# Kernel tuning notes

Hardware: AMD Instinct MI355X
Metric: run time of the kernel (lower is better)

## Reference

```python
import jax, jax.numpy as jnp
import numpy as np
from jax import lax

H = 16        # linear_num_key_heads == linear_num_value_heads
DK = 64       # linear_key_head_dim
DV = 128      # linear_value_head_dim
HID = 2048    # hidden_size
KCONV = 4     # linear_conv_kernel_dim
SEQ = 2048
KEY_DIM = H * DK       # 1024
VAL_DIM = H * DV       # 2048
CONV_DIM = 2 * KEY_DIM + VAL_DIM  # 4096


def _l2norm(x, eps=1e-6):
    return x * lax.rsqrt(jnp.sum(x * x, axis=-1, keepdims=True) + eps)


def setup_inputs() -> dict:
    key = jax.random.key(0)
    ks = jax.random.split(key, 10)
    s = 0.02
    return {
        "hidden_states": jax.random.normal(ks[0], (1, SEQ, HID), jnp.float32),
        "in_proj_qkv": jax.random.normal(ks[1], (CONV_DIM, HID), jnp.float32) * s,
        "in_proj_a": jax.random.normal(ks[2], (H, HID), jnp.float32) * s,
        "in_proj_b": jax.random.normal(ks[3], (H, HID), jnp.float32) * s,
        "in_proj_z": jax.random.normal(ks[4], (VAL_DIM, HID), jnp.float32) * s,
        "conv_w": jax.random.normal(ks[5], (CONV_DIM, 1, KCONV), jnp.float32) * 0.5,
        "A_log": jax.random.normal(ks[6], (H,), jnp.float32) * 0.5,
        "dt_bias": jnp.ones((H,), jnp.float32),
        "norm_w": jnp.ones((DV,), jnp.float32),
        "out_proj": jax.random.normal(ks[7], (HID, VAL_DIM), jnp.float32) * s,
        "is_prefill": 1,
    }


def reference(hidden_states, in_proj_qkv, in_proj_a, in_proj_b, in_proj_z,
              conv_w, A_log, dt_bias, norm_w, out_proj, is_prefill):
    b, s, _ = hidden_states.shape  # b == 1
    # QKV projection: (1, S, CONV_DIM)
    mixed = jnp.einsum('bsh,oh->bso', hidden_states, in_proj_qkv)
    # Depthwise causal conv1d over time (left pad K-1), then SiLU
    x = mixed.transpose(0, 2, 1)  # (1, C, S)
    x = lax.conv_general_dilated(
        x, conv_w, window_strides=(1,), padding=[(KCONV - 1, 0)],
        feature_group_count=CONV_DIM, dimension_numbers=('NCH', 'OIH', 'NCH'))
    mixed = jax.nn.silu(x).transpose(0, 2, 1)[0]  # (S, CONV_DIM), squeeze batch

    q = mixed[:, :KEY_DIM].reshape(s, H, DK)
    k = mixed[:, KEY_DIM:2 * KEY_DIM].reshape(s, H, DK)
    v = mixed[:, 2 * KEY_DIM:].reshape(s, H, DV)

    hs = hidden_states[0]  # (S, HID)
    a = hs @ in_proj_a.T                      # (S, H)
    g = -jnp.exp(A_log) * jax.nn.softplus(a + dt_bias)  # (S, H) log-decay
    beta = jax.nn.sigmoid(hs @ in_proj_b.T)   # (S, H)
    z = (hs @ in_proj_z.T).reshape(s, H, DV)  # (S, H, DV)

    q = _l2norm(q) * (1.0 / np.sqrt(DK))
    k = _l2norm(k)

    # Delta-rule recurrence; prefill -> zero initial state
    S0 = jnp.zeros((H, DK, DV), jnp.float32)

    def step(St, inp):
        q_t, k_t, v_t, g_t, beta_t = inp
        St = St * jnp.exp(g_t)[:, None, None]            # decay
        kv_mem = jnp.einsum('hk,hkv->hv', k_t, St)       # read
        delta = (v_t - kv_mem) * beta_t[:, None]         # gated error
        St = St + jnp.einsum('hk,hv->hkv', k_t, delta)   # rank-1 update
        o_t = jnp.einsum('hk,hkv->hv', q_t, St)          # query read
        return St, o_t

    _, core = lax.scan(step, S0, (q, k, v, g, beta))  # core: (S, H, DV)

    # Gated RMSNorm over DV, then SiLU(z) gate
    var = jnp.mean(core * core, axis=-1, keepdims=True)
    core = core * lax.rsqrt(var + 1e-6) * norm_w
    core = core * jax.nn.silu(z)
    core = core.reshape(1, s, VAL_DIM)
    return jnp.einsum('bsv,hv->bsh', core, out_proj)
```

## Files before the change

### kernel.cpp

```cpp
#include <hip/hip_runtime.h>
#include <stdint.h>


#define SEQ 2048
#define HIDDEN 2048
#define NH 16
#define DKv 64
#define DVv 128
#define KEY_DIM 1024
#define VAL_DIM 2048
#define CONV_DIM 4096

typedef __bf16 bf16;
typedef unsigned short u16;
typedef __attribute__((ext_vector_type(8))) __bf16 bf16x8;
typedef __attribute__((ext_vector_type(4))) __bf16 bf16x4;
typedef __attribute__((ext_vector_type(4))) float f32x4;

#define AS1 __attribute__((address_space(1)))
#define AS3 __attribute__((address_space(3)))
#define GLDS16(src, dst) __builtin_amdgcn_global_load_lds((AS1 const void*)(src), (AS3 void*)(dst), 16, 0, 0)

__device__ __forceinline__ float b2f(u16 u) {
  union { unsigned int i; float f; } c; c.i = ((unsigned int)u) << 16; return c.f;
}
__device__ __forceinline__ float sigmoidf_(float x) { return 1.0f / (1.0f + __expf(-x)); }

__global__ void detect_dtype(const u16* __restrict__ p, unsigned* __restrict__ flag) {
  int lane = threadIdx.x;
  int cnt = 0;
  for (int w = lane; w < 2048; w += 64) {
    unsigned e = (p[2 * w] >> 7) & 0xFF;
    if (e < 64) cnt++;
  }
  cnt += __shfl_xor(cnt, 1);  cnt += __shfl_xor(cnt, 2);  cnt += __shfl_xor(cnt, 4);
  cnt += __shfl_xor(cnt, 8);  cnt += __shfl_xor(cnt, 16); cnt += __shfl_xor(cnt, 32);
  if (lane == 0) *flag = (cnt > 64) ? 1u : 0u;
}

__global__ __launch_bounds__(256)
void cvt_bf16(const void* __restrict__ src, bf16* __restrict__ dst, long n,
              const unsigned* __restrict__ flagp) {
  long i = ((long)blockIdx.x * 256 + threadIdx.x) * 8;
  if (i >= n) return;
  if (*flagp) {
    const f32x4* s = (const f32x4*)((const float*)src + i);
    f32x4 a = s[0], b = s[1];
    bf16x8 o;
#pragma unroll
    for (int j = 0; j < 4; ++j) { o[j] = (bf16)a[j]; o[4 + j] = (bf16)b[j]; }
    *(bf16x8*)(dst + i) = o;
  } else {
    *(bf16x8*)(dst + i) = *(const bf16x8*)((const bf16*)src + i);
  }
}

template<bool F32OUT>
__global__ __launch_bounds__(256, 2)
void gemm_nt(const void* __restrict__ Araw, const void* __restrict__ Braw,
             void* __restrict__ Cv, int N, int K,
             const unsigned* __restrict__ flagp, int useA, int useB) {
  __shared__ __align__(16) bf16 As[128 * 32];
  __shared__ __align__(16) bf16 Bs[128 * 32];
  const bool f32g = (*flagp != 0);
  const bool fA = useA && f32g;
  const bool fB = useB && f32g;
  const int tid  = threadIdx.x;
  const int lane = tid & 63;
  const int wv   = tid >> 6;
  const int wm   = (wv & 1) << 6;
  const int wn   = (wv >> 1) << 6;
  const long bm  = (long)blockIdx.y * 128;
  const long bn  = (long)blockIdx.x * 128;

  f32x4 acc[4][4] = {};

  for (int k0 = 0; k0 < K; k0 += 32) {
#pragma unroll
    for (int it = 0; it < 2; ++it) {
      int e   = (it * 256 + tid) * 8;
      int row = e >> 5;
      int col = e & 31;
      long offA = (bm + row) * (long)K + (k0 + col);
      long offB = (bn + row) * (long)K + (k0 + col);
      if (fA) {
        const float* g = (const float*)Araw + offA;
        f32x4 u0 = *(const f32x4*)g, u1 = *(const f32x4*)(g + 4);
        bf16x8 bv;
#pragma unroll
        for (int j = 0; j < 4; ++j) { bv[j] = (bf16)u0[j]; bv[4 + j] = (bf16)u1[j]; }
        *(bf16x8*)&As[e] = bv;
      } else {
        const bf16* g = (const bf16*)Araw + offA;
        GLDS16(g, &As[e]);
      }
      if (fB) {
        const float* g = (const float*)Braw + offB;
        f32x4 u0 = *(const f32x4*)g, u1 = *(const f32x4*)(g + 4);
        bf16x8 bv;
#pragma unroll
        for (int j = 0; j < 4; ++j) { bv[j] = (bf16)u0[j]; bv[4 + j] = (bf16)u1[j]; }
        *(bf16x8*)&Bs[e] = bv;
      } else {
        const bf16* g = (const bf16*)Braw + offB;
        GLDS16(g, &Bs[e]);
      }
    }
    __syncthreads();

    const bf16x8* As8 = (const bf16x8*)As;
    const bf16x8* Bs8 = (const bf16x8*)Bs;
    const int r = lane & 15, q = lane >> 4;
    bf16x8 af[4], bfr[4];
#pragma unroll
    for (int i = 0; i < 4; ++i) af[i]  = As8[(wm + i * 16 + r) * 4 + q];
#pragma unroll
    for (int j = 0; j < 4; ++j) bfr[j] = Bs8[(wn + j * 16 + r) * 4 + q];
#pragma unroll
    for (int i = 0; i < 4; ++i)
#pragma unroll
      for (int j = 0; j < 4; ++j)
        acc[i][j] = __builtin_amdgcn_mfma_f32_16x16x32_bf16(af[i], bfr[j], acc[i][j], 0, 0, 0);
    __syncthreads();
  }

  const int r = lane & 15, q = lane >> 4;
#pragma unroll
  for (int i = 0; i < 4; ++i)
#pragma unroll
    for (int j = 0; j < 4; ++j) {
      long row = bm + wm + i * 16 + q * 4;
      long col = bn + wn + j * 16 + r;
#pragma unroll
      for (int rr = 0; rr < 4; ++rr) {
        if constexpr (F32OUT) ((float*)Cv)[(row + rr) * N + col] = acc[i][j][rr];
        else                  ((bf16*)Cv)[(row + rr) * N + col] = (bf16)acc[i][j][rr];
      }
    }
}

__device__ void gemm_body_bf16(char* smemc, const bf16* __restrict__ A,
                               const bf16* __restrict__ B, bf16* __restrict__ C,
                               int N, int K, int bx, int by, int tid) {
  bf16* As = (bf16*)smemc;
  bf16* Bs = (bf16*)(smemc + 8192);
  const int lane = tid & 63;
  const int wv = tid >> 6, wm = (wv & 1) << 6, wn = (wv >> 1) << 6;
  const long bm = (long)by * 128, bn = (long)bx * 128;
  f32x4 acc[4][4] = {};
  for (int k0 = 0; k0 < K; k0 += 32) {
#pragma unroll
    for (int it = 0; it < 2; ++it) {
      int e = (it * 256 + tid) * 8;
      int row = e >> 5, col = e & 31;
      const bf16* gA = A + (bm + row) * (long)K + k0 + col;
      const bf16* gB = B + (bn + row) * (long)K + k0 + col;
      GLDS16(gA, &As[e]);
      GLDS16(gB, &Bs[e]);
    }
    __syncthreads();
    const bf16x8* As8 = (const bf16x8*)As;
    const bf16x8* Bs8 = (const bf16x8*)Bs;
    const int r = lane & 15, q = lane >> 4;
    bf16x8 af[4], bfr[4];
#pragma unroll
    for (int i = 0; i < 4; ++i) af[i]  = As8[(wm + i * 16 + r) * 4 + q];
#pragma unroll
    for (int j = 0; j < 4; ++j) bfr[j] = Bs8[(wn + j * 16 + r) * 4 + q];
#pragma unroll
    for (int i = 0; i < 4; ++i)
#pragma unroll
      for (int j = 0; j < 4; ++j)
        acc[i][j] = __builtin_amdgcn_mfma_f32_16x16x32_bf16(af[i], bfr[j], acc[i][j], 0, 0, 0);
    __syncthreads();
  }
  const int r = lane & 15, q = lane >> 4;
#pragma unroll
  for (int i = 0; i < 4; ++i)
#pragma unroll
    for (int j = 0; j < 4; ++j) {
      long row = bm + wm + i * 16 + q * 4;
      long col = bn + wn + j * 16 + r;
#pragma unroll
      for (int rr = 0; rr < 4; ++rr)
        C[(row + rr) * (long)N + col] = (bf16)acc[i][j][rr];
    }
}

__global__ __launch_bounds__(256)
void proj_ab(const void* __restrict__ hsr, const void* __restrict__ War,
             const void* __restrict__ Wbr, const void* __restrict__ A_logr,
             const void* __restrict__ dtbr,
             float* __restrict__ eg, float* __restrict__ bet,
             float* __restrict__ gb,
             const unsigned* __restrict__ flagp) {
  const bool f32g = (*flagp != 0);
  const int s = blockIdx.x;
  const int t = threadIdx.x;
  const int o = t & 31;
  const int part = t >> 5;
  const int h = o & 15;
  const int kbeg = part * 256;
  float a0 = 0.f, a1 = 0.f;
  if (f32g) {
    const f32x4* x4 = (const f32x4*)((const float*)hsr + (long)s * HIDDEN + kbeg);
    const f32x4* w4 = (const f32x4*)((const float*)((o < 16) ? War : Wbr) + (long)h * HIDDEN + kbeg);
#pragma unroll 8
    for (int k4 = 0; k4 < 64; ++k4) {
      f32x4 xv = x4[k4], wv = w4[k4];
      a0 += xv[0] * wv[0] + xv[1] * wv[1];
      a1 += xv[2] * wv[2] + xv[3] * wv[3];
    }
  } else {
    const bf16x8* x8 = (const bf16x8*)((const bf16*)hsr + (long)s * HIDDEN + kbeg);
    const bf16x8* w8 = (const bf16x8*)((const bf16*)((o < 16) ? War : Wbr) + (long)h * HIDDEN + kbeg);
#pragma unroll 8
    for (int k8 = 0; k8 < 32; ++k8) {
      bf16x8 xv = x8[k8], wv = w8[k8];
#pragma unroll
      for (int j = 0; j < 4; ++j) a0 += (float)xv[j] * (float)wv[j];
#pragma unroll
      for (int j = 4; j < 8; ++j) a1 += (float)xv[j] * (float)wv[j];
    }
  }
  __shared__ float red[256];
  red[t] = a0 + a1;
  __syncthreads();
  if (t < 32) {
    float a = 0.f;
#pragma unroll
    for (int p = 0; p < 8; ++p) a += red[t + p * 32];
    const int hh = t & 15;
    if (t < 16) {
      float alog = f32g ? ((const float*)A_logr)[hh] : b2f(((const u16*)A_logr)[hh]);
      float dtb  = f32g ? ((const float*)dtbr)[hh]   : b2f(((const u16*)dtbr)[hh]);
      float xx = a + dtb;
      float sp = fmaxf(xx, 0.f) + log1pf(__expf(-fabsf(xx)));
      float gg = -__expf(alog) * sp;
      if (gb) gb[(long)s * NH + hh] = gg;
      eg[(long)s * NH + hh] = __expf(gg);
    } else {
      bet[(long)s * NH + hh] = sigmoidf_(a);
    }
  }
}

__global__ __launch_bounds__(256)
void conv_norm(const bf16* __restrict__ mixed, const void* __restrict__ convwr,
               bf16* __restrict__ qbuf, bf16* __restrict__ kbuf, bf16* __restrict__ vbuf,
               const unsigned* __restrict__ flagp) {
  const bool f32g = (*flagp != 0);
  const int s = blockIdx.x;
  const int c = blockIdx.y * 256 + threadIdx.x;
  float w0, w1, w2, w3;
  if (f32g) {
    const float* wp = (const float*)convwr + (long)c * 4;
    w0 = wp[0]; w1 = wp[1]; w2 = wp[2]; w3 = wp[3];
  } else {
    const u16* wp = (const u16*)convwr + (long)c * 4;
    w0 = b2f(wp[0]); w1 = b2f(wp[1]); w2 = b2f(wp[2]); w3 = b2f(wp[3]);
  }
  float acc = w3 * (float)mixed[(long)s * CONV_DIM + c];
  if (s >= 1) acc += w2 * (float)mixed[(long)(s - 1) * CONV_DIM + c];
  if (s >= 2) acc += w1 * (float)mixed[(long)(s - 2) * CONV_DIM + c];
  if (s >= 3) acc += w0 * (float)mixed[(long)(s - 3) * CONV_DIM + c];
  float y = acc * sigmoidf_(acc);
  if (c < 2 * KEY_DIM) {
    float ss = y * y;
    ss += __shfl_xor(ss, 1);  ss += __shfl_xor(ss, 2);  ss += __shfl_xor(ss, 4);
    ss += __shfl_xor(ss, 8);  ss += __shfl_xor(ss, 16); ss += __shfl_xor(ss, 32);
    float scale = rsqrtf(ss + 1e-6f);
    if (c < KEY_DIM) scale *= 0.125f;
    y *= scale;
  }
  if (c < KEY_DIM)            qbuf[(long)s * KEY_DIM + c] = (bf16)y;
  else if (c < 2 * KEY_DIM)   kbuf[(long)s * KEY_DIM + (c - KEY_DIM)] = (bf16)y;
  else                        vbuf[(long)s * VAL_DIM + (c - 2 * KEY_DIM)] = (bf16)y;
}

template<int CTRL>
__device__ __forceinline__ float dpp_add(float x) {
  int y = __builtin_amdgcn_update_dpp(0, __float_as_int(x), CTRL, 0xF, 0xF, true);
  return x + __int_as_float(y);
}
__device__ __forceinline__ float dpp_sum16(float x) {
  x = dpp_add<0xB1>(x);
  x = dpp_add<0x4E>(x);
  x = dpp_add<0x141>(x);
  x = dpp_add<0x140>(x);
  return x;
}

__global__ __launch_bounds__(256, 2)
void fused_scan(const bf16* __restrict__ qbuf, const bf16* __restrict__ kbuf,
                const bf16* __restrict__ vbuf, const float* __restrict__ eg,
                const float* __restrict__ bet, bf16* __restrict__ core,
                const bf16* __restrict__ hsb, const bf16* __restrict__ wzb,
                bf16* __restrict__ zbuf, const void* __restrict__ woutr,
                bf16* __restrict__ woutb, const unsigned* __restrict__ flagp,
                int nScan, int nGemm) {
  __shared__ __align__(16) char smem[16384];
  const int t = threadIdx.x;
  const int b = blockIdx.x;

  if (b < nScan) {
    const int h  = b >> 3;
    const int vg = (b & 7) * 16;
    const int g  = t >> 4;
    const int L  = t & 15;
    bf16*  kqs = (bf16*)smem;
    bf16*  vts = (bf16*)(smem + 8192);
    float* ets = (float*)(smem + 9216);
    float* bts = (float*)(smem + 9344);

#define STAGE(buf, s0)                                                          \
    {                                                                           \
      int byte = t * 16;                                                        \
      const bf16* src;                                                          \
      if (byte < 2048) {                                                        \
        int row = byte >> 7, el = (byte & 127) >> 1;                            \
        src = kbuf + (long)((s0) + row) * KEY_DIM + h * DKv + el;               \
      } else {                                                                  \
        int b2 = byte - 2048;                                                   \
        int row = b2 >> 7, el = (b2 & 127) >> 1;                                \
        src = qbuf + (long)((s0) + row) * KEY_DIM + h * DKv + el;               \
      }                                                                         \
      GLDS16(src, smem + (buf) * 4096 + byte);                                  \
      if (t < 32) {                                                             \
        int row = t >> 1, el = (t & 1) * 8;                                     \
        const bf16* vsrc = vbuf + (long)((s0) + row) * VAL_DIM + h * DVv + vg + el; \
        GLDS16(vsrc, smem + 8192 + (buf) * 512 + t * 16);                       \
      }                                                                         \
    }

    float er = 0.f, br = 0.f;
    if (t < 16)      er = eg[(long)t * NH + h];
    else if (t < 32) br = bet[(long)(t - 16) * NH + h];
    STAGE(0, 0);
    if (t < 16)      ets[t] = er;
    else if (t < 32) bts[t - 16] = br;
    __syncthreads();

    float S0 = 0.f, S1 = 0.f, S2 = 0.f, S3 = 0.f;
    for (int tile = 0; tile < 128; ++tile) {
      const int buf = tile & 1, nb = buf ^ 1;
      if (tile < 127) {
        STAGE(nb, (tile + 1) * 16);
        if (t < 16)      er = eg[(long)((tile + 1) * 16 + t) * NH + h];
        else if (t < 32) br = bet[(long)((tile + 1) * 16 + (t - 16)) * NH + h];
      }
      const bf16*  ktb = kqs + buf * 2048;
      const bf16*  qtb = ktb + 1024;
      const bf16*  vtb = vts + buf * 256;
      const float* etb = ets + buf * 16;
      const float* btb = bts + buf * 16;
      const long sbase = (long)tile * 16;

      bf16x4 kR[2], qR[2];
      float  vR[2], eR[2], bR[2];
      kR[0] = *(const bf16x4*)(ktb + 0 * 64 + L * 4);
      qR[0] = *(const bf16x4*)(qtb + 0 * 64 + L * 4);
      vR[0] = (float)vtb[0 * 16 + g];  eR[0] = etb[0];  bR[0] = btb[0];
      kR[1] = *(const bf16x4*)(ktb + 1 * 64 + L * 4);
      qR[1] = *(const bf16x4*)(qtb + 1 * 64 + L * 4);
      vR[1] = (float)vtb[1 * 16 + g];  eR[1] = etb[1];  bR[1] = btb[1];
#pragma unroll
      for (int s = 0; s < 16; ++s) {
        const int sl = s & 1;
        bf16x4 kk = kR[sl], qq = qR[sl];
        float vv = vR[sl], ee = eR[sl], bb = bR[sl];
        if (s < 14) {
          const int s2 = s + 2;
          kR[sl] = *(const bf16x4*)(ktb + s2 * 64 + L * 4);
          qR[sl] = *(const bf16x4*)(qtb + s2 * 64 + L * 4);
          vR[sl] = (float)vtb[s2 * 16 + g];
          eR[sl] = etb[s2];  bR[sl] = btb[s2];
        }
        float ebt = ee * bb, vbt = vv * bb;
        float k0 = (float)kk[0], k1 = (float)kk[1], k2 = (float)kk[2], k3 = (float)kk[3];
        float D0 = S0 * ee, D1 = S1 * ee, D2 = S2 * ee, D3 = S3 * ee;
        float p = (k0 * S0 + k1 * S1) + (k2 * S2 + k3 * S3);
        p = dpp_sum16(p);
        float delta = vbt - ebt * p;
        S0 = fmaf(k0, delta, D0); S1 = fmaf(k1, delta, D1);
        S2 = fmaf(k2, delta, D2); S3 = fmaf(k3, delta, D3);
        float q0 = (float)qq[0], q1 = (float)qq[1], q2 = (float)qq[2], q3 = (float)qq[3];
        float o = (q0 * S0 + q1 * S1) + (q2 * S2 + q3 * S3);
        o = dpp_sum16(o);
        if (L == 0) core[(sbase + s) * VAL_DIM + h * DVv + vg + g] = (bf16)o;
      }
      if (tile < 127) {
        if (t < 16)      ets[nb * 16 + t] = er;
        else if (t < 32) bts[nb * 16 + (t - 16)] = br;
      }
      __syncthreads();
    }
#undef STAGE
  } else if (b < nScan + nGemm) {
    int gb = b - nScan;
    gemm_body_bf16(smem, hsb, wzb, zbuf, VAL_DIM, HIDDEN, gb & 15, gb >> 4, t);
  } else {
    long i = ((long)(b - nScan - nGemm) * 256 + t) * 8;
    if (i < (long)HIDDEN * VAL_DIM) {
      if (*flagp) {
        const f32x4* s = (const f32x4*)((const float*)woutr + i);
        f32x4 a = s[0], c = s[1];
        bf16x8 o;
#pragma unroll
        for (int j = 0; j < 4; ++j) { o[j] = (bf16)a[j]; o[4 + j] = (bf16)c[j]; }
        *(bf16x8*)(woutb + i) = o;
      } else {
        *(bf16x8*)(woutb + i) = *(const bf16x8*)((const bf16*)woutr + i);
      }
    }
  }
}


__global__ __launch_bounds__(256, 2)
void chunk_a(const bf16* __restrict__ kbuf, const bf16* __restrict__ vbuf,
             const float* __restrict__ gbuf, const float* __restrict__ betp,
             bf16* __restrict__ dloc, bf16* __restrict__ whig, bf16* __restrict__ wlog,
             const bf16* __restrict__ hsb, const bf16* __restrict__ wzb,
             bf16* __restrict__ zbuf, const void* __restrict__ woutr,
             bf16* __restrict__ woutb, const unsigned* __restrict__ flagp) {
  __shared__ __align__(16) char smem[25600];
  const int t = threadIdx.x;
  const int b = blockIdx.x;
  if (b < 512) {
    const int c = b >> 4, h = b & 15;
    bf16*  Ks   = (bf16*)smem;
    float* At   = (float*)(smem + 8192);
    float* cumS = (float*)(smem + 24576);
    float* bS   = (float*)(smem + 24832);
    float* dS   = (float*)(smem + 25088);
#pragma unroll
    for (int it = 0; it < 2; ++it) {
      int byte = (it * 256 + t) * 16;
      int row = byte >> 7, col = (byte & 127) >> 1;
      const bf16* src = kbuf + (long)(c * 64 + row) * KEY_DIM + h * DKv + col;
      GLDS16(src, smem + byte);
    }
    if (t < 64) {
      float cc = gbuf[(long)(c * 64 + t) * NH + h];
#pragma unroll
      for (int d = 1; d < 64; d <<= 1) { float y = __shfl_up(cc, d); if (t >= d) cc += y; }
      cumS[t] = cc;
      dS[t] = __expf(cc);
      bS[t] = betp[(long)(c * 64 + t) * NH + h];
    }
    {
      f32x4 z = {0.f, 0.f, 0.f, 0.f};
#pragma unroll
      for (int i = 0; i < 4; ++i) ((f32x4*)At)[t * 4 + i] = z;
    }
    __syncthreads();
    {
      const int lane = t & 63, wv = t >> 6;
      const int r = lane & 15, q = lane >> 4;
      const bf16x8* Ks8 = (const bf16x8*)Ks;
#pragma unroll
      for (int n = 0; n < 4; ++n) {
        f32x4 acc = {0.f, 0.f, 0.f, 0.f};
#pragma unroll
        for (int kk = 0; kk < 2; ++kk) {
          bf16x8 af  = Ks8[(wv * 16 + r) * 8 + kk * 4 + q];
          bf16x8 bfv = Ks8[(n  * 16 + r) * 8 + kk * 4 + q];
          acc = __builtin_amdgcn_mfma_f32_16x16x32_bf16(af, bfv, acc, 0, 0, 0);
        }
        const int i = n * 16 + r;
#pragma unroll
        for (int rr = 0; rr < 4; ++rr) {
          const int tr = wv * 16 + q * 4 + rr;
          if (i < tr)
            At[i * 64 + tr] = bS[tr] * __expf(cumS[tr] - cumS[i]) * acc[rr];
        }
      }
    }
    __syncthreads();
    if (t < 192) {
      float x[64];
      const long base = ((long)(c * 16 + h)) * 64;
      if (t < 128) {
#pragma unroll
        for (int s = 0; s < 64; ++s)
          x[s] = bS[s] * (float)vbuf[(long)(c * 64 + s) * VAL_DIM + h * DVv + t];
      } else {
        const int k = t - 128;
#pragma unroll
        for (int s = 0; s < 64; ++s)
          x[s] = bS[s] * dS[s] * (float)Ks[s * 64 + k];
      }
#pragma unroll
      for (int s = 0; s < 64; ++s) {
        const float val = x[s];
        const f32x4* row4 = (const f32x4*)(At + s * 64);
#pragma unroll
        for (int qd = (s >> 2); qd < 16; ++qd) {
          f32x4 a4 = row4[qd];
          x[qd * 4 + 0] = fmaf(-a4[0], val, x[qd * 4 + 0]);
          x[qd * 4 + 1] = fmaf(-a4[1], val, x[qd * 4 + 1]);
          x[qd * 4 + 2] = fmaf(-a4[2], val, x[qd * 4 + 2]);
          x[qd * 4 + 3] = fmaf(-a4[3], val, x[qd * 4 + 3]);
        }
      }
      if (t < 128) {
#pragma unroll
        for (int s = 0; s < 64; ++s)
          dloc[(base + s) * 128 + t] = (bf16)x[s];
      } else {
        const int k = t - 128;
        const long wb = base * 64;
#pragma unroll
        for (int s = 0; s < 64; ++s) {
          float v = -x[s];
          bf16 hh = (bf16)v;
          whig[wb + s * 64 + k] = hh;
          wlog[wb + s * 64 + k] = (bf16)(v - (float)hh);
        }
      }
    }
  } else if (b < 768) {
    int gb = b - 512;
    gemm_body_bf16(smem, hsb, wzb, zbuf, VAL_DIM, HIDDEN, gb & 15, gb >> 4, t);
  } else {
    long i = ((long)(b - 768) * 256 + t) * 8;
    if (i < (long)HIDDEN * VAL_DIM) {
      if (*flagp) {
        const f32x4* s = (const f32x4*)((const float*)woutr + i);
        f32x4 a = s[0], cc = s[1];
        bf16x8 o;
#pragma unroll
        for (int j = 0; j < 4; ++j) { o[j] = (bf16)a[j]; o[4 + j] = (bf16)cc[j]; }
        *(bf16x8*)(woutb + i) = o;
      } else {
        *(bf16x8*)(woutb + i) = *(const bf16x8*)((const bf16*)woutr + i);
      }
    }
  }
}

__global__ __launch_bounds__(256, 1)
void chunk_b(const bf16* __restrict__ qbuf, const bf16* __restrict__ kbuf,
             const float* __restrict__ gbuf, const bf16* __restrict__ dloc,
             const bf16* __restrict__ whig, const bf16* __restrict__ wlog,
             bf16* __restrict__ dTg, bf16* __restrict__ o1g) {
  __shared__ __align__(16) char smem[123904];
  bf16* Wh  = (bf16*)(smem);
  bf16* Wl  = (bf16*)(smem + 16384);
  bf16* Qs  = (bf16*)(smem + 32768);
  bf16* Ks  = (bf16*)(smem + 49152);
  bf16* Dls = (bf16*)(smem + 65536);
  bf16* KT  = (bf16*)(smem + 81920);
  bf16* Shi = (bf16*)(smem + 90112);
  bf16* Slo = (bf16*)(smem + 98304);
  bf16* Dth = (bf16*)(smem + 106496);
  bf16* Dtl = (bf16*)(smem + 114688);
  float* fSb = (float*)(smem + 122880);
  float* dSb = (float*)(smem + 123392);

  const int t = threadIdx.x;
  const int h = blockIdx.x >> 1, vhalf = blockIdx.x & 1;
  const int lane = t & 63, w = t >> 6;
  const int r = lane & 15, q = lane >> 4;
  const int tb = w * 16 + q * 4;

  auto stage = [&](int bb, int cc) {
    const long c16h = (long)(cc * 16 + h);
#pragma unroll
    for (int it = 0; it < 2; ++it) {
      int p = it * 256 + t;
      int row = p >> 3, g = p & 7;
      int sg = ((g ^ (row & 7)) << 3);
      GLDS16(whig + c16h * 4096 + row * 64 + sg, (char*)Wh + bb * 8192 + p * 16);
      GLDS16(wlog + c16h * 4096 + row * 64 + sg, (char*)Wl + bb * 8192 + p * 16);
      GLDS16(qbuf + (long)(cc * 64 + row) * KEY_DIM + h * DKv + sg, (char*)Qs + bb * 8192 + p * 16);
      GLDS16(kbuf + (long)(cc * 64 + row) * KEY_DIM + h * DKv + (g << 3), (char*)Ks + bb * 8192 + p * 16);
      GLDS16(dloc + (c16h * 64 + row) * 128 + vhalf * 64 + sg, (char*)Dls + bb * 8192 + p * 16);
    }
  };
  auto prefix = [&](int bb, int cc) {
    if (t < 64) {
      float cs = gbuf[(long)(cc * 64 + t) * NH + h];
#pragma unroll
      for (int d = 1; d < 64; d <<= 1) { float y = __shfl_up(cs, d); if (t >= d) cs += y; }
      float tot = __shfl(cs, 63);
      fSb[bb * 64 + t] = __expf(tot - cs);
      dSb[bb * 64 + t] = __expf(cs);
    }
  };

  {
    f32x4 z = {0.f, 0.f, 0.f, 0.f};
    ((f32x4*)Shi)[t] = z; ((f32x4*)Shi)[t + 256] = z;
    ((f32x4*)Slo)[t] = z; ((f32x4*)Slo)[t + 256] = z;
  }
  stage(0, 0);
  prefix(0, 0);
  f32x4 Sacc[4] = {};

  for (int c = 0; c < 32; ++c) {
    const int buf = c & 1, nb = buf ^ 1;
    __syncthreads();
    const bf16* wh = Wh + buf * 4096;
    const bf16* wl = Wl + buf * 4096;
    const bf16* qs = Qs + buf * 4096;
    const bf16* ks = Ks + buf * 4096;
    const bf16* dl = Dls + buf * 4096;
    const float* fS = fSb + buf * 64;
    const float* dS = dSb + buf * 64;
    const long gch = (long)(c * 16 + h) * 8192 + (long)(vhalf * 64) * 64;

    if (c < 31) {
      const int k = lane;
#pragma unroll
      for (int ii = 0; ii < 16; ++ii) {
        const int i = w * 16 + ii;
        const int pg = (i >> 3) ^ (k & 7);
        KT[k * 64 + pg * 8 + (i & 7)] = ks[i * 64 + k];
      }
    }

    float fs4[4], ds4[4];
#pragma unroll
    for (int rr = 0; rr < 4; ++rr) { fs4[rr] = fS[tb + rr]; ds4[rr] = dS[tb + rr]; }

    bf16x8 wahi[2], walo[2], qa[2];
#pragma unroll
    for (int kk = 0; kk < 2; ++kk) {
      const int row = w * 16 + r;
      const int g = (kk * 4 + q) ^ (row & 7);
      wahi[kk] = *(const bf16x8*)(wh + row * 64 + g * 8);
      walo[kk] = *(const bf16x8*)(wl + row * 64 + g * 8);
      qa[kk]   = *(const bf16x8*)(qs + row * 64 + g * 8);
    }

#pragma unroll
    for (int n = 0; n < 4; ++n) {
      const int vrow = n * 16 + r;
      bf16x8 sh[2], sl[2];
#pragma unroll
      for (int kk = 0; kk < 2; ++kk) {
        const int g = (kk * 4 + q) ^ (vrow & 7);
        sh[kk] = *(const bf16x8*)(Shi + vrow * 64 + g * 8);
        sl[kk] = *(const bf16x8*)(Slo + vrow * 64 + g * 8);
      }
      f32x4 da;
#pragma unroll
      for (int rr = 0; rr < 4; ++rr) {
        const int trow = tb + rr;
        const int pg = (vrow >> 3) ^ (trow & 7);
        da[rr] = (float)dl[trow * 64 + pg * 8 + (vrow & 7)];
      }
      f32x4 oa = {0.f, 0.f, 0.f, 0.f};
#pragma unroll
      for (int kk = 0; kk < 2; ++kk) {
        da = __builtin_amdgcn_mfma_f32_16x16x32_bf16(wahi[kk], sh[kk], da, 0, 0, 0);
        da = __builtin_amdgcn_mfma_f32_16x16x32_bf16(wahi[kk], sl[kk], da, 0, 0, 0);
        da = __builtin_amdgcn_mfma_f32_16x16x32_bf16(walo[kk], sh[kk], da, 0, 0, 0);
        oa = __builtin_amdgcn_mfma_f32_16x16x32_bf16(qa[kk],   sh[kk], oa, 0, 0, 0);
        oa = __builtin_amdgcn_mfma_f32_16x16x32_bf16(qa[kk],   sl[kk], oa, 0, 0, 0);
      }
      bf16x4 dpk, opk, fhk, flk;
#pragma unroll
      for (int rr = 0; rr < 4; ++rr) {
        float dv = da[rr];
        dpk[rr] = (bf16)dv;
        float p = fs4[rr] * dv;
        bf16 ph = (bf16)p;
        fhk[rr] = ph;
        flk[rr] = (bf16)(p - (float)ph);
        opk[rr] = (bf16)(ds4[rr] * oa[rr]);
      }
      *(bf16x4*)(dTg + gch + (long)vrow * 64 + tb) = dpk;
      *(bf16x4*)(o1g + gch + (long)vrow * 64 + tb) = opk;
      const int pg = (tb >> 3) ^ (vrow & 7);
      *(bf16x4*)(Dth + vrow * 64 + pg * 8 + (tb & 7)) = fhk;
      *(bf16x4*)(Dtl + vrow * 64 + pg * 8 + (tb & 7)) = flk;
    }

    __syncthreads();
    if (c < 31) {
      stage(nb, c + 1);
      prefix(nb, c + 1);
      const float dC = dS[63];
      bf16x8 dh[2], dlo[2];
#pragma unroll
      for (int kk = 0; kk < 2; ++kk) {
        const int vrow = w * 16 + r;
        const int g = (kk * 4 + q) ^ (vrow & 7);
        dh[kk]  = *(const bf16x8*)(Dth + vrow * 64 + g * 8);
        dlo[kk] = *(const bf16x8*)(Dtl + vrow * 64 + g * 8);
      }
#pragma unroll
      for (int n = 0; n < 4; ++n) {
        f32x4 sa;
#pragma unroll
        for (int rr = 0; rr < 4; ++rr) sa[rr] = dC * Sacc[n][rr];
        bf16x8 ktf[2];
#pragma unroll
        for (int kk = 0; kk < 2; ++kk) {
          const int krow = n * 16 + r;
          const int g = (kk * 4 + q) ^ (krow & 7);
          ktf[kk] = *(const bf16x8*)(KT + krow * 64 + g * 8);
        }
#pragma unroll
        for (int kk = 0; kk < 2; ++kk) {
          sa = __builtin_amdgcn_mfma_f32_16x16x32_bf16(dh[kk],  ktf[kk], sa, 0, 0, 0);
          sa = __builtin_amdgcn_mfma_f32_16x16x32_bf16(dlo[kk], ktf[kk], sa, 0, 0, 0);
        }
        Sacc[n] = sa;
        const int k = n * 16 + r;
#pragma unroll
        for (int rr = 0; rr < 4; ++rr) {
          const int v = tb + rr;
          float s = sa[rr];
          bf16 hh = (bf16)s;
          const int pg = (k >> 3) ^ (v & 7);
          Shi[v * 64 + pg * 8 + (k & 7)] = hh;
          Slo[v * 64 + pg * 8 + (k & 7)] = (bf16)(s - (float)hh);
        }
      }
    }
  }
}

__global__ __launch_bounds__(256, 2)
void chunk_c(const bf16* __restrict__ qbuf, const bf16* __restrict__ kbuf,
             const float* __restrict__ gbuf, const bf16* __restrict__ dTg,
             const bf16* __restrict__ o1g, bf16* __restrict__ core) {
  __shared__ __align__(16) char smem[57600];
  const int t = threadIdx.x;
  const int c = blockIdx.x >> 4, h = blockIdx.x & 15;
  const long c16h = (long)(c * 16 + h);
  bf16* Qs  = (bf16*)smem;
  bf16* Ksl = (bf16*)(smem + 8192);
  bf16* Pl  = (bf16*)(smem + 16384);
  const bf16* dT  = (const bf16*)(smem + 24576);
  const bf16* o1l = (const bf16*)(smem + 40960);
  float* cumS = (float*)(smem + 57344);

#pragma unroll
  for (int it = 0; it < 2; ++it) {
    int byte = (it * 256 + t) * 16;
    int row = byte >> 7, col = (byte & 127) >> 1;
    GLDS16(qbuf + (long)(c * 64 + row) * KEY_DIM + h * DKv + col, smem + byte);
    GLDS16(kbuf + (long)(c * 64 + row) * KEY_DIM + h * DKv + col, smem + 8192 + byte);
  }
#pragma unroll
  for (int it = 0; it < 4; ++it) {
    int byte = (it * 256 + t) * 16;
    GLDS16(dTg + c16h * 8192 + (byte >> 1), smem + 24576 + byte);
    GLDS16(o1g + c16h * 8192 + (byte >> 1), smem + 40960 + byte);
  }
  if (t < 64) {
    float cc = gbuf[(long)(c * 64 + t) * NH + h];
#pragma unroll
    for (int d = 1; d < 64; d <<= 1) { float y = __shfl_up(cc, d); if (t >= d) cc += y; }
    cumS[t] = cc;
  }
  __syncthreads();

  const int lane = t & 63, wv = t >> 6;
  const int r = lane & 15, q = lane >> 4;
  const bf16x8* Qs8 = (const bf16x8*)Qs;
  const bf16x8* Ks8 = (const bf16x8*)Ksl;

#pragma unroll
  for (int n = 0; n < 4; ++n) {
    f32x4 acc = {0.f, 0.f, 0.f, 0.f};
#pragma unroll
    for (int kk = 0; kk < 2; ++kk)
      acc = __builtin_amdgcn_mfma_f32_16x16x32_bf16(
          Qs8[(wv * 16 + r) * 8 + kk * 4 + q], Ks8[(n * 16 + r) * 8 + kk * 4 + q], acc, 0, 0, 0);
    const int i = n * 16 + r;
#pragma unroll
    for (int rr = 0; rr < 4; ++rr) {
      const int tr = wv * 16 + q * 4 + rr;
      Pl[tr * 64 + i] = (i <= tr) ? (bf16)(__expf(cumS[tr] - cumS[i]) * acc[rr]) : (bf16)0.0f;
    }
  }
  __syncthreads();

  {
    const bf16x8* Pl8 = (const bf16x8*)Pl;
    const bf16x8* dT8 = (const bf16x8*)dT;
    bf16x8 pf[2];
#pragma unroll
    for (int kk = 0; kk < 2; ++kk) pf[kk] = Pl8[(wv * 16 + r) * 8 + kk * 4 + q];
#pragma unroll
    for (int n = 0; n < 8; ++n) {
      const int v = n * 16 + r;
      f32x4 acc;
#pragma unroll
      for (int rr = 0; rr < 4; ++rr)
        acc[rr] = (float)o1l[v * 64 + (wv * 16 + q * 4 + rr)];
#pragma unroll
      for (int kk = 0; kk < 2; ++kk)
        acc = __builtin_amdgcn_mfma_f32_16x16x32_bf16(
            pf[kk], dT8[(n * 16 + r) * 8 + kk * 4 + q], acc, 0, 0, 0);
#pragma unroll
      for (int rr = 0; rr < 4; ++rr) {
        const int tr = wv * 16 + q * 4 + rr;
        core[(long)(c * 64 + tr) * VAL_DIM + h * DVv + v] = (bf16)acc[rr];
      }
    }
  }
}

__global__ __launch_bounds__(256)
void gate_norm(const bf16* __restrict__ core, const bf16* __restrict__ zb,
               const void* __restrict__ normwr, bf16* __restrict__ gated,
               const unsigned* __restrict__ flagp) {
  const bool f32g = (*flagp != 0);
  const int s  = blockIdx.x;
  const int t  = threadIdx.x;
  const int h  = t >> 4;
  const int li = t & 15;
  const long base = (long)s * VAL_DIM + h * DVv + li * 8;
  bf16x8 c8 = *(const bf16x8*)(core + base);
  bf16x8 z8 = *(const bf16x8*)(zb + base);
  float x[8], z[8], nw[8];
  float ss = 0.f;
#pragma unroll
  for (int j = 0; j < 8; ++j) { x[j] = (float)c8[j]; z[j] = (float)z8[j]; ss += x[j] * x[j]; }
  if (f32g) {
    const float* np_ = (const float*)normwr + li * 8;
#pragma unroll
    for (int j = 0; j < 8; ++j) nw[j] = np_[j];
  } else {
    const u16* np_ = (const u16*)normwr + li * 8;
#pragma unroll
    for (int j = 0; j < 8; ++j) nw[j] = b2f(np_[j]);
  }
  ss += __shfl_xor(ss, 1); ss += __shfl_xor(ss, 2);
  ss += __shfl_xor(ss, 4); ss += __shfl_xor(ss, 8);
  float scale = rsqrtf(ss * (1.f / 128.f) + 1e-6f);
#pragma unroll
  for (int j = 0; j < 8; ++j) {
    float y = x[j] * scale * nw[j];
    y *= z[j] * sigmoidf_(z[j]);
    gated[base + j] = (bf16)y;
  }
}

extern "C" void kernel_launch(void* const* d_in, const int* in_sizes, int n_in,
                              void* d_out, int out_size, void* d_ws, size_t ws_size,
                              hipStream_t stream) {
  char* ws = (char*)d_ws;
  const bool big = ws_size >= ((48u << 20) + (512u << 10));

  if (big) {
    bf16*  hsb   = (bf16*)ws;
    bf16*  wqkvb = (bf16*)(ws + (8u << 20));
    bf16*  wzb   = (bf16*)(ws + (8u << 20));
    bf16*  zbuf  = (bf16*)(ws + (16u << 20));
    bf16*  mixed = (bf16*)(ws + (24u << 20));
    bf16*  whig  = (bf16*)(ws + (24u << 20));
    bf16*  wlog  = (bf16*)(ws + (28u << 20));
    bf16*  woutb = (bf16*)(ws + (32u << 20));
    bf16*  qbuf  = (bf16*)(ws + (40u << 20));
    bf16*  kbuf  = (bf16*)(ws + (44u << 20));
    bf16*  gated = (bf16*)(ws + (40u << 20));
    bf16*  dTg   = (bf16*)ws;
    bf16*  o1g   = (bf16*)(ws + (8u << 20));
    float* egp  = (float*)(ws + (48u << 20));
    float* betp = (float*)(ws + (48u << 20) + (128u << 10));
    float* gbp  = (float*)(ws + (48u << 20) + (256u << 10));
    unsigned* flagp = (unsigned*)(ws + (48u << 20) + (384u << 10));
    bf16* vbuf  = (bf16*)d_out;
    bf16* dlocp = (bf16*)((char*)d_out + (8u << 20));
    bf16* corep = (bf16*)d_out;

    detect_dtype<<<1, 64, 0, stream>>>((const u16*)d_in[0], flagp);
    proj_ab<<<SEQ, 256, 0, stream>>>(d_in[0], d_in[2], d_in[3], d_in[6], d_in[7], egp, betp, gbp, flagp);
    cvt_bf16<<<(SEQ * HIDDEN) / 2048, 256, 0, stream>>>(d_in[0], hsb, (long)SEQ * HIDDEN, flagp);
    cvt_bf16<<<(CONV_DIM * HIDDEN) / 2048, 256, 0, stream>>>(d_in[1], wqkvb, (long)CONV_DIM * HIDDEN, flagp);
    gemm_nt<false><<<dim3(CONV_DIM / 128, SEQ / 128), 256, 0, stream>>>(hsb, wqkvb, mixed, CONV_DIM, HIDDEN, flagp, 0, 0);
    cvt_bf16<<<(VAL_DIM * HIDDEN) / 2048, 256, 0, stream>>>(d_in[4], wzb, (long)VAL_DIM * HIDDEN, flagp);
    conv_norm<<<dim3(SEQ, CONV_DIM / 256), 256, 0, stream>>>(mixed, d_in[5], qbuf, kbuf, vbuf, flagp);
    chunk_a<<<512 + 256 + 2048, 256, 0, stream>>>(kbuf, vbuf, gbp, betp, dlocp, whig, wlog,
                                                  hsb, wzb, zbuf, d_in[9], woutb, flagp);
    chunk_b<<<32, 256, 0, stream>>>(qbuf, kbuf, gbp, dlocp, whig, wlog, dTg, o1g);
    chunk_c<<<512, 256, 0, stream>>>(qbuf, kbuf, gbp, dTg, o1g, corep);
    gate_norm<<<SEQ, 256, 0, stream>>>(corep, zbuf, d_in[8], gated, flagp);
    gemm_nt<true><<<dim3(HIDDEN / 128, SEQ / 128), 256, 0, stream>>>(gated, woutb, d_out, HIDDEN, VAL_DIM, flagp, 0, 0);
  } else {
    bf16* mixed = (bf16*)ws;
    bf16* qbuf  = (bf16*)(ws + (16u << 20));
    bf16* kbuf  = (bf16*)(ws + (20u << 20));
    bf16* zbuf  = (bf16*)ws;
    bf16* corep = (bf16*)(ws + (8u << 20));
    bf16* gated = (bf16*)(ws + (16u << 20));
    float* egp  = (float*)(ws + (24u << 20));
    float* betp = (float*)(ws + (24u << 20) + (128u << 10));
    unsigned* flagp = (unsigned*)(ws + (24u << 20) + (256u << 10));
    bf16* vbuf  = (bf16*)d_out;

    detect_dtype<<<1, 64, 0, stream>>>((const u16*)d_in[0], flagp);
    proj_ab<<<SEQ, 256, 0, stream>>>(d_in[0], d_in[2], d_in[3], d_in[6], d_in[7], egp, betp, nullptr, flagp);
    gemm_nt<false><<<dim3(CONV_DIM / 128, SEQ / 128), 256, 0, stream>>>(d_in[0], d_in[1], mixed, CONV_DIM, HIDDEN, flagp, 1, 1);
    conv_norm<<<dim3(SEQ, CONV_DIM / 256), 256, 0, stream>>>(mixed, d_in[5], qbuf, kbuf, vbuf, flagp);
    gemm_nt<false><<<dim3(VAL_DIM / 128, SEQ / 128), 256, 0, stream>>>(d_in[0], d_in[4], zbuf, VAL_DIM, HIDDEN, flagp, 1, 1);
    fused_scan<<<128, 256, 0, stream>>>(qbuf, kbuf, vbuf, egp, betp, corep,
                                        nullptr, nullptr, nullptr, nullptr, nullptr, flagp,
                                        128, 0);
    gate_norm<<<SEQ, 256, 0, stream>>>(corep, zbuf, d_in[8], gated, flagp);
    gemm_nt<true><<<dim3(HIDDEN / 128, SEQ / 128), 256, 0, stream>>>(gated, d_in[9], d_out, HIDDEN, VAL_DIM, flagp, 0, 1);
  }
}
```

Baseline: 531.7 us.

## Precompute all chunk decay prefixes upfront, issue next-chunk staging earlier, batch LDS loads

```diff
diff --git a/kernel.cpp b/kernel.cpp
--- a/kernel.cpp
+++ b/kernel.cpp
@@ -545,7 +545,7 @@
              const float* __restrict__ gbuf, const bf16* __restrict__ dloc,
              const bf16* __restrict__ whig, const bf16* __restrict__ wlog,
              bf16* __restrict__ dTg, bf16* __restrict__ o1g) {
-  __shared__ __align__(16) char smem[123904];
+  __shared__ __align__(16) char smem[139264];
   bf16* Wh  = (bf16*)(smem);
   bf16* Wl  = (bf16*)(smem + 16384);
   bf16* Qs  = (bf16*)(smem + 32768);
@@ -556,8 +556,8 @@
   bf16* Slo = (bf16*)(smem + 98304);
   bf16* Dth = (bf16*)(smem + 106496);
   bf16* Dtl = (bf16*)(smem + 114688);
-  float* fSb = (float*)(smem + 122880);
-  float* dSb = (float*)(smem + 123392);
+  float* fSa = (float*)(smem + 122880);
+  float* dSa = (float*)(smem + 131072);
 
   const int t = threadIdx.x;
   const int h = blockIdx.x >> 1, vhalf = blockIdx.x & 1;
@@ -579,36 +579,41 @@
       GLDS16(dloc + (c16h * 64 + row) * 128 + vhalf * 64 + sg, (char*)Dls + bb * 8192 + p * 16);
     }
   };
-  auto prefix = [&](int bb, int cc) {
-    if (t < 64) {
-      float cs = gbuf[(long)(cc * 64 + t) * NH + h];
-#pragma unroll
-      for (int d = 1; d < 64; d <<= 1) { float y = __shfl_up(cs, d); if (t >= d) cs += y; }
+
+  {
+    float g8[8];
+#pragma unroll
+    for (int i = 0; i < 8; ++i)
+      g8[i] = gbuf[(long)((w * 8 + i) * 64 + lane) * NH + h];
+#pragma unroll
+    for (int i = 0; i < 8; ++i) {
+      float cs = g8[i];
+#pragma unroll
+      for (int d = 1; d < 64; d <<= 1) { float y = __shfl_up(cs, d); if (lane >= d) cs += y; }
       float tot = __shfl(cs, 63);
-      fSb[bb * 64 + t] = __expf(tot - cs);
-      dSb[bb * 64 + t] = __expf(cs);
-    }
-  };
-
+      fSa[(w * 8 + i) * 64 + lane] = __expf(tot - cs);
+      dSa[(w * 8 + i) * 64 + lane] = __expf(cs);
+    }
+  }
   {
     f32x4 z = {0.f, 0.f, 0.f, 0.f};
     ((f32x4*)Shi)[t] = z; ((f32x4*)Shi)[t + 256] = z;
     ((f32x4*)Slo)[t] = z; ((f32x4*)Slo)[t + 256] = z;
   }
   stage(0, 0);
-  prefix(0, 0);
   f32x4 Sacc[4] = {};
 
   for (int c = 0; c < 32; ++c) {
     const int buf = c & 1, nb = buf ^ 1;
     __syncthreads();
+    if (c < 31) stage(nb, c + 1);
     const bf16* wh = Wh + buf * 4096;
     const bf16* wl = Wl + buf * 4096;
     const bf16* qs = Qs + buf * 4096;
     const bf16* ks = Ks + buf * 4096;
     const bf16* dl = Dls + buf * 4096;
-    const float* fS = fSb + buf * 64;
-    const float* dS = dSb + buf * 64;
+    const float* fS = fSa + c * 64;
+    const float* dS = dSa + c * 64;
     const long gch = (long)(c * 16 + h) * 8192 + (long)(vhalf * 64) * 64;
 
     if (c < 31) {
@@ -634,43 +639,51 @@
       walo[kk] = *(const bf16x8*)(wl + row * 64 + g * 8);
       qa[kk]   = *(const bf16x8*)(qs + row * 64 + g * 8);
     }
+    bf16x8 sh[4][2], sl[4][2];
+#pragma unroll
+    for (int n = 0; n < 4; ++n)
+#pragma unroll
+      for (int kk = 0; kk < 2; ++kk) {
+        const int vrow = n * 16 + r;
+        const int g = (kk * 4 + q) ^ (vrow & 7);
+        sh[n][kk] = *(const bf16x8*)(Shi + vrow * 64 + g * 8);
+        sl[n][kk] = *(const bf16x8*)(Slo + vrow * 64 + g * 8);
+      }
+    float dl4[4][4];
+#pragma unroll
+    for (int n = 0; n < 4; ++n)
+#pragma unroll
+      for (int rr = 0; rr < 4; ++rr) {
+        const int vrow = n * 16 + r, trow = tb + rr;
+        const int pg = (vrow >> 3) ^ (trow & 7);
+        dl4[n][rr] = (float)dl[trow * 64 + pg * 8 + (vrow & 7)];
+      }
+
+    f32x4 da[4] = {}, oa[4] = {};
+#pragma unroll
+    for (int n = 0; n < 4; ++n)
+#pragma unroll
+      for (int kk = 0; kk < 2; ++kk) {
+        da[n] = __builtin_amdgcn_mfma_f32_16x16x32_bf16(wahi[kk], sh[n][kk], da[n], 0, 0, 0);
+        da[n] = __builtin_amdgcn_mfma_f32_16x16x32_bf16(wahi[kk], sl[n][kk], da[n], 0, 0, 0);
+        da[n] = __builtin_amdgcn_mfma_f32_16x16x32_bf16(walo[kk], sh[n][kk], da[n], 0, 0, 0);
+        oa[n] = __builtin_amdgcn_mfma_f32_16x16x32_bf16(qa[kk],   sh[n][kk], oa[n], 0, 0, 0);
+        oa[n] = __builtin_amdgcn_mfma_f32_16x16x32_bf16(qa[kk],   sl[n][kk], oa[n], 0, 0, 0);
+      }
 
 #pragma unroll
     for (int n = 0; n < 4; ++n) {
       const int vrow = n * 16 + r;
-      bf16x8 sh[2], sl[2];
-#pragma unroll
-      for (int kk = 0; kk < 2; ++kk) {
-        const int g = (kk * 4 + q) ^ (vrow & 7);
-        sh[kk] = *(const bf16x8*)(Shi + vrow * 64 + g * 8);
-        sl[kk] = *(const bf16x8*)(Slo + vrow * 64 + g * 8);
-      }
-      f32x4 da;
+      bf16x4 dpk, opk, fhk, flk;
 #pragma unroll
       for (int rr = 0; rr < 4; ++rr) {
-        const int trow = tb + rr;
-        const int pg = (vrow >> 3) ^ (trow & 7);
-        da[rr] = (float)dl[trow * 64 + pg * 8 + (vrow & 7)];
-      }
-      f32x4 oa = {0.f, 0.f, 0.f, 0.f};
-#pragma unroll
-      for (int kk = 0; kk < 2; ++kk) {
-        da = __builtin_amdgcn_mfma_f32_16x16x32_bf16(wahi[kk], sh[kk], da, 0, 0, 0);
-        da = __builtin_amdgcn_mfma_f32_16x16x32_bf16(wahi[kk], sl[kk], da, 0, 0, 0);
-        da = __builtin_amdgcn_mfma_f32_16x16x32_bf16(walo[kk], sh[kk], da, 0, 0, 0);
-        oa = __builtin_amdgcn_mfma_f32_16x16x32_bf16(qa[kk],   sh[kk], oa, 0, 0, 0);
-        oa = __builtin_amdgcn_mfma_f32_16x16x32_bf16(qa[kk],   sl[kk], oa, 0, 0, 0);
-      }
-      bf16x4 dpk, opk, fhk, flk;
-#pragma unroll
-      for (int rr = 0; rr < 4; ++rr) {
-        float dv = da[rr];
+        float dv = dl4[n][rr] + da[n][rr];
         dpk[rr] = (bf16)dv;
         float p = fs4[rr] * dv;
         bf16 ph = (bf16)p;
         fhk[rr] = ph;
         flk[rr] = (bf16)(p - (float)ph);
-        opk[rr] = (bf16)(ds4[rr] * oa[rr]);
+        opk[rr] = (bf16)(ds4[rr] * oa[n][rr]);
       }
       *(bf16x4*)(dTg + gch + (long)vrow * 64 + tb) = dpk;
       *(bf16x4*)(o1g + gch + (long)vrow * 64 + tb) = opk;
@@ -681,33 +694,32 @@
 
     __syncthreads();
     if (c < 31) {
-      stage(nb, c + 1);
-      prefix(nb, c + 1);
       const float dC = dS[63];
-      bf16x8 dh[2], dlo[2];
+      bf16x8 dh[2], dlo2[2], ktf[4][2];
 #pragma unroll
       for (int kk = 0; kk < 2; ++kk) {
         const int vrow = w * 16 + r;
         const int g = (kk * 4 + q) ^ (vrow & 7);
-        dh[kk]  = *(const bf16x8*)(Dth + vrow * 64 + g * 8);
-        dlo[kk] = *(const bf16x8*)(Dtl + vrow * 64 + g * 8);
-      }
-#pragma unroll
-      for (int n = 0; n < 4; ++n) {
-        f32x4 sa;
-#pragma unroll
-        for (int rr = 0; rr < 4; ++rr) sa[rr] = dC * Sacc[n][rr];
-        bf16x8 ktf[2];
+        dh[kk]   = *(const bf16x8*)(Dth + vrow * 64 + g * 8);
+        dlo2[kk] = *(const bf16x8*)(Dtl + vrow * 64 + g * 8);
+      }
+#pragma unroll
+      for (int n = 0; n < 4; ++n)
 #pragma unroll
         for (int kk = 0; kk < 2; ++kk) {
           const int krow = n * 16 + r;
           const int g = (kk * 4 + q) ^ (krow & 7);
-          ktf[kk] = *(const bf16x8*)(KT + krow * 64 + g * 8);
+          ktf[n][kk] = *(const bf16x8*)(KT + krow * 64 + g * 8);
         }
 #pragma unroll
+      for (int n = 0; n < 4; ++n) {
+        f32x4 sa;
+#pragma unroll
+        for (int rr = 0; rr < 4; ++rr) sa[rr] = dC * Sacc[n][rr];
+#pragma unroll
         for (int kk = 0; kk < 2; ++kk) {
-          sa = __builtin_amdgcn_mfma_f32_16x16x32_bf16(dh[kk],  ktf[kk], sa, 0, 0, 0);
-          sa = __builtin_amdgcn_mfma_f32_16x16x32_bf16(dlo[kk], ktf[kk], sa, 0, 0, 0);
+          sa = __builtin_amdgcn_mfma_f32_16x16x32_bf16(dh[kk],   ktf[n][kk], sa, 0, 0, 0);
+          sa = __builtin_amdgcn_mfma_f32_16x16x32_bf16(dlo2[kk], ktf[n][kk], sa, 0, 0, 0);
         }
         Sacc[n] = sa;
         const int k = n * 16 + r;
```

Result: faster. 503.2 us (-5.4%).
